# Performance work log

Hardware: AMD Instinct MI355X
Metric: run time of the kernel (lower is better)

Reference implementation:

```python
import jax, jax.numpy as jnp
import numpy as np

MAX_FPS = 30.0
NUM_HEADS = 8


def _rope(x, times):
    # x: [B, H, T, D] with D even; interleaved rotary (even/odd pairs)
    B, H, T, D = x.shape
    inv_freq = 1.0 / (10000.0 ** (jnp.arange(0, D, 2, dtype=jnp.float32) / D))  # [D/2]
    pos = jnp.round(times * MAX_FPS)                       # [B, T]
    freqs = pos[:, :, None] * inv_freq[None, None, :]      # [B, T, D/2]
    cos = jnp.cos(freqs)[:, None, :, :]                    # [B, 1, T, D/2]
    sin = jnp.sin(freqs)[:, None, :, :]
    xp = x.reshape(B, H, T, D // 2, 2)
    x0, x1 = xp[..., 0], xp[..., 1]                        # even-index, odd-index elems
    r0 = x0 * cos - x1 * sin
    r1 = x0 * sin + x1 * cos
    return jnp.stack([r0, r1], axis=-1).reshape(B, H, T, D)


def setup_inputs() -> dict:
    key = jax.random.key(0)
    k1, k2, k3, k4, k5 = jax.random.split(key, 5)
    B, N, C = 4, 2048, 512
    x = jax.random.normal(k1, (B, N, C), dtype=jnp.float32)
    mask = jnp.zeros((B, N), dtype=jnp.float32)  # additive mask, 0 = attend
    # times in seconds; rounded to frame indices inside RoPE
    times = jax.random.uniform(k2, (B, N), dtype=jnp.float32) * (N / MAX_FPS)
    bound_qkv = float(np.sqrt(6.0 / (C + 3 * C)))
    Wqkv = jax.random.uniform(k3, (3 * C, C), minval=-bound_qkv, maxval=bound_qkv, dtype=jnp.float32)
    bound_p = float(np.sqrt(6.0 / (C + C)))
    Wproj = jax.random.uniform(k4, (C, C), minval=-bound_p, maxval=bound_p, dtype=jnp.float32)
    bproj = jnp.zeros((C,), dtype=jnp.float32)
    return {"x": x, "mask": mask, "times": times, "Wqkv": Wqkv,
            "Wproj": Wproj, "bproj": bproj, "num_cls_token": 0}


def reference(x, mask, times, Wqkv, Wproj, bproj, num_cls_token):
    B, N, C = x.shape
    H = NUM_HEADS
    Dh = C // H
    qkv = (x @ Wqkv.T).reshape(B, N, 3, H, Dh).transpose(2, 0, 3, 1, 4)  # [3,B,H,N,Dh]
    q, k, v = qkv[0], qkv[1], qkv[2]
    if num_cls_token > 0:
        c_q, q = q[:, :, :num_cls_token], q[:, :, num_cls_token:]
        c_k, k = k[:, :, :num_cls_token], k[:, :, num_cls_token:]
        t = times
        q = _rope(q, t)
        k = _rope(k, t)
        q = jnp.concatenate([c_q, q], axis=2)
        k = jnp.concatenate([c_k, k], axis=2)
    else:
        q = _rope(q, times)
        k = _rope(k, times)
    scale = 1.0 / jnp.sqrt(jnp.float32(Dh))
    scores = jnp.einsum('bhqd,bhkd->bhqk', q, k) * scale + mask[:, None, None, :]
    attn = jax.nn.softmax(scores, axis=-1)
    out = jnp.einsum('bhqk,bhkd->bhqd', attn, v)           # [B,H,N,Dh]
    out = out.transpose(0, 2, 1, 3).reshape(B, N, C)
    return out @ Wproj.T + bproj
```

## Files before the change

kernel.cpp:

```cpp
#include <hip/hip_runtime.h>
#include <math.h>

#define BB 4
#define NN 2048
#define CC 512
#define HH 8
#define DH 64
#define MM (BB*NN)
#define QKV_N (3*CC)

typedef _Float16 f16;
typedef __attribute__((ext_vector_type(4))) _Float16 f16x4;
typedef __attribute__((ext_vector_type(8))) _Float16 f16x8;
typedef __attribute__((ext_vector_type(4))) float f32x4;

#define L2E 1.4426950408889634f

#define GL16(g, l) __builtin_amdgcn_global_load_lds(                       \
    (const __attribute__((address_space(1))) void*)(g),                    \
    (__attribute__((address_space(3))) void*)(l), 16, 0, 0)

#define SX4 (MM*CC/4)
#define SW4 (QKV_N*CC/4)
#define SP4 (CC*CC/4)
__global__ __launch_bounds__(256) void cast_kernel(
    const float* __restrict__ x, const float* __restrict__ wqkv,
    const float* __restrict__ wproj,
    f16* __restrict__ xh, f16* __restrict__ wqh, f16* __restrict__ wph)
{
    const int t = blockIdx.x * 256 + threadIdx.x;
    const float* src; f16* dst; int i;
    if (t < SX4)            { src = x;     dst = xh;  i = t; }
    else if (t < SX4 + SW4) { src = wqkv;  dst = wqh; i = t - SX4; }
    else                    { src = wproj; dst = wph; i = t - SX4 - SW4; }
    f32x4 v = *(const f32x4*)(src + 4 * (size_t)i);
    f16x4 h = { (f16)v[0], (f16)v[1], (f16)v[2], (f16)v[3] };
    *(f16x4*)(dst + 4 * (size_t)i) = h;
}

__global__ __launch_bounds__(256) void qkv_gemm(
    const f16* __restrict__ xh, const f16* __restrict__ wh,
    f16* __restrict__ qo, f16* __restrict__ ko, f16* __restrict__ vto)
{
    __shared__ f16 As[128][32];
    __shared__ f16 Bs[128][32];
    const int m0 = blockIdx.x * 128;
    const int n0 = blockIdx.y * 128;
    const int tid = threadIdx.x;
    const int lane = tid & 63;
    const int w = tid >> 6;
    const int wm = (w & 1) * 64, wn = (w >> 1) * 64;
    const int l15 = lane & 15, quad = lane >> 4;

    const int sr = tid >> 2;
    const int sc = (tid & 3) * 8;
    const f16* ga0 = xh + (size_t)(m0 + sr) * CC + sc;
    const f16* ga1 = xh + (size_t)(m0 + sr + 64) * CC + sc;
    const f16* gb0 = wh + (size_t)(n0 + sr) * CC + sc;
    const f16* gb1 = wh + (size_t)(n0 + sr + 64) * CC + sc;
    f16* la0 = &As[sr][sc];      f16* la1 = &As[sr + 64][sc];
    f16* lb0 = &Bs[sr][sc];      f16* lb1 = &Bs[sr + 64][sc];

    f32x4 acc[4][4] = {};
    for (int k0 = 0; k0 < CC; k0 += 32) {
        __syncthreads();
        GL16(ga0 + k0, la0);
        GL16(ga1 + k0, la1);
        GL16(gb0 + k0, lb0);
        GL16(gb1 + k0, lb1);
        __syncthreads();

        f16x8 af[4], bf[4];
        #pragma unroll
        for (int mi = 0; mi < 4; ++mi)
            af[mi] = *(const f16x8*)&As[wm + mi*16 + l15][quad * 8];
        #pragma unroll
        for (int ni = 0; ni < 4; ++ni)
            bf[ni] = *(const f16x8*)&Bs[wn + ni*16 + l15][quad * 8];
        #pragma unroll
        for (int mi = 0; mi < 4; ++mi)
            #pragma unroll
            for (int ni = 0; ni < 4; ++ni)
                acc[mi][ni] = __builtin_amdgcn_mfma_f32_16x16x32_f16(
                    af[mi], bf[ni], acc[mi][ni], 0, 0, 0);
    }

    const int which = n0 >> 9;
    const int b     = m0 >> 11;
    const int mloc  = m0 & (NN - 1);

    if (which == 2) {
        #pragma unroll
        for (int mi = 0; mi < 4; ++mi)
            #pragma unroll
            for (int ni = 0; ni < 4; ++ni) {
                const int cl = wn + ni*16 + l15;
                const int hh = ((n0 & 511) + cl) >> 6;
                const int d  = ((n0 & 511) + cl) & 63;
                const int n  = mloc + wm + mi*16 + quad*4;
                f16x4 pk = { (f16)acc[mi][ni][0], (f16)acc[mi][ni][1],
                             (f16)acc[mi][ni][2], (f16)acc[mi][ni][3] };
                *(f16x4*)(vto + ((size_t)(b*HH + hh) * DH + d) * NN + n) = pk;
            }
        return;
    }

    f16* dst = which ? ko : qo;
    #pragma unroll
    for (int mi = 0; mi < 4; ++mi)
        #pragma unroll
        for (int r = 0; r < 4; ++r) {
            const int n = mloc + wm + mi*16 + quad*4 + r;
            #pragma unroll
            for (int ni = 0; ni < 4; ++ni) {
                const int cl = wn + ni*16 + l15;
                const int hh = ((n0 & 511) + cl) >> 6;
                const int d  = ((n0 & 511) + cl) & 63;
                dst[((size_t)(b*HH + hh) * NN + n) * DH + d] = (f16)acc[mi][ni][r];
            }
        }
}

__global__ __launch_bounds__(256) void rope_kernel(
    f16* __restrict__ q, f16* __restrict__ k,
    const float* __restrict__ times, const int* __restrict__ nclsp)
{
    const int t = blockIdx.x * 256 + threadIdx.x;
    const int row = t >> 3;
    const int d0  = (t & 7) * 8;
    const int n   = row & (NN - 1);
    const int b   = row >> 14;
    if (n < *nclsp) return;
    const float pos = rintf(times[b * NN + n] * 30.0f);

    f16x8 qv = *(const f16x8*)(q + (size_t)row * DH + d0);
    f16x8 kv = *(const f16x8*)(k + (size_t)row * DH + d0);
    f16x8 qr, kr;
    #pragma unroll
    for (int p = 0; p < 4; ++p) {
        const int j = (d0 >> 1) + p;
        const float invf = exp2f((float)j * (-13.287712379549449f / 32.0f));
        float s, c;
        sincosf(pos * invf, &s, &c);
        const float q0 = (float)qv[2*p], q1 = (float)qv[2*p+1];
        qr[2*p]   = (f16)(q0 * c - q1 * s);
        qr[2*p+1] = (f16)(q0 * s + q1 * c);
        const float k0 = (float)kv[2*p], k1 = (float)kv[2*p+1];
        kr[2*p]   = (f16)(k0 * c - k1 * s);
        kr[2*p+1] = (f16)(k0 * s + k1 * c);
    }
    *(f16x8*)(q + (size_t)row * DH + d0) = qr;
    *(f16x8*)(k + (size_t)row * DH + d0) = kr;
}

__global__ __launch_bounds__(256, 2) void attn_kernel(
    const f16* __restrict__ qg, const f16* __restrict__ kg,
    const f16* __restrict__ vtg, const float* __restrict__ mask,
    f16* __restrict__ out)
{
    __shared__ f16 Kh[64][64];
    __shared__ f16 Vt[64][64];
    __shared__ float Msk[64];

    const int bh = blockIdx.x;
    const int qt = blockIdx.y;
    const int b = bh >> 3, h = bh & 7;
    const int tid = threadIdx.x;
    const int w = tid >> 6, lane = tid & 63;
    const int l15 = lane & 15, quad = lane >> 4;
    const int rho = l15 & 7;

    const f16* qbase  = qg  + ((size_t)bh * NN + qt*128 + w*32) * DH;
    const f16* kbase  = kg  + (size_t)bh * NN * DH;
    const f16* vtbase = vtg + (size_t)bh * DH * NN;
    const float* mbase = mask + (size_t)b * NN;

    f16x8 Bq[2][2];
    #pragma unroll
    for (int ni = 0; ni < 2; ++ni)
        #pragma unroll
        for (int kc = 0; kc < 2; ++kc)
            Bq[ni][kc] = *(const f16x8*)(qbase + (size_t)(16*ni + l15) * DH
                                         + kc*32 + quad*8);

    const f16x4 Aones = (l15 == 0) ? f16x4{1.0f16, 1.0f16, 1.0f16, 1.0f16}
                                   : f16x4{0.0f16, 0.0f16, 0.0f16, 0.0f16};

    f32x4 O[2][4] = {};
    f32x4 Lacc[2] = {};
    float m_run[2] = { -INFINITY, -INFINITY };
    const float scl = 0.125f * L2E;

    const int srr = tid >> 3;
    const int scb = tid & 7;
    const int sw  = (scb ^ (srr & 7)) * 8;

    for (int kt = 0; kt < 32; ++kt) {
        __syncthreads();
        f16x8 k0 = *(const f16x8*)(kbase + (size_t)(kt*64 + srr) * DH + scb*8);
        f16x8 k1 = *(const f16x8*)(kbase + (size_t)(kt*64 + srr + 32) * DH + scb*8);
        f16x8 v0 = *(const f16x8*)(vtbase + (size_t)srr * NN + kt*64 + scb*8);
        f16x8 v1 = *(const f16x8*)(vtbase + (size_t)(srr + 32) * NN + kt*64 + scb*8);
        *(f16x8*)&Kh[srr][sw]      = k0;
        *(f16x8*)&Kh[srr + 32][sw] = k1;
        *(f16x8*)&Vt[srr][sw]      = v0;
        *(f16x8*)&Vt[srr + 32][sw] = v1;
        if (tid < 16) {
            f32x4 mv = *(const f32x4*)(mbase + kt*64 + (tid << 2));
            mv *= L2E;
            *(f32x4*)&Msk[tid << 2] = mv;
        }
        __syncthreads();

        f32x4 st[4][2] = {};
        const int aw = (quad ^ rho) * 8;
        #pragma unroll
        for (int mi = 0; mi < 4; ++mi) {
            f16x8 Ak0 = *(const f16x8*)&Kh[16*mi + l15][aw];
            f16x8 Ak1 = *(const f16x8*)&Kh[16*mi + l15][aw ^ 32];
            #pragma unroll
            for (int ni = 0; ni < 2; ++ni) {
                st[mi][ni] = __builtin_amdgcn_mfma_f32_16x16x32_f16(Ak0, Bq[ni][0], st[mi][ni], 0, 0, 0);
                st[mi][ni] = __builtin_amdgcn_mfma_f32_16x16x32_f16(Ak1, Bq[ni][1], st[mi][ni], 0, 0, 0);
            }
        }

        f32x4 mskv[4];
        #pragma unroll
        for (int mi = 0; mi < 4; ++mi)
            mskv[mi] = *(const f32x4*)&Msk[16*mi + quad*4];

        f16x4 ph[4][2];
        float alpha[2];
        #pragma unroll
        for (int ni = 0; ni < 2; ++ni) {
            float mloc = -INFINITY;
            #pragma unroll
            for (int mi = 0; mi < 4; ++mi)
                #pragma unroll
                for (int r = 0; r < 4; ++r) {
                    float s2 = st[mi][ni][r] * scl + mskv[mi][r];
                    st[mi][ni][r] = s2;
                    mloc = fmaxf(mloc, s2);
                }
            mloc = fmaxf(mloc, __shfl_xor(mloc, 16));
            mloc = fmaxf(mloc, __shfl_xor(mloc, 32));
            const float mnew = fmaxf(m_run[ni], mloc);
            alpha[ni] = exp2f(m_run[ni] - mnew);
            m_run[ni] = mnew;
            #pragma unroll
            for (int mi = 0; mi < 4; ++mi)
                #pragma unroll
                for (int r = 0; r < 4; ++r)
                    ph[mi][ni][r] = (f16)exp2f(st[mi][ni][r] - mnew);
            #pragma unroll
            for (int nd = 0; nd < 4; ++nd)
                O[ni][nd] *= alpha[ni];
            Lacc[ni] *= alpha[ni];
        }

        #pragma unroll
        for (int mi = 0; mi < 4; ++mi) {
            Lacc[0] = __builtin_amdgcn_mfma_f32_16x16x16f16(Aones, ph[mi][0], Lacc[0], 0, 0, 0);
            Lacc[1] = __builtin_amdgcn_mfma_f32_16x16x16f16(Aones, ph[mi][1], Lacc[1], 0, 0, 0);
            #pragma unroll
            for (int nd = 0; nd < 4; ++nd) {
                const int vb = ((2*mi + (quad >> 1)) ^ rho) * 8 + (quad & 1) * 4;
                f16x4 Av = *(const f16x4*)&Vt[16*nd + l15][vb];
                O[0][nd] = __builtin_amdgcn_mfma_f32_16x16x16f16(Av, ph[mi][0], O[0][nd], 0, 0, 0);
                O[1][nd] = __builtin_amdgcn_mfma_f32_16x16x16f16(Av, ph[mi][1], O[1][nd], 0, 0, 0);
            }
        }
    }

    #pragma unroll
    for (int ni = 0; ni < 2; ++ni) {
        const float l = __shfl(Lacc[ni][0], l15);
        const float inv = 1.0f / l;
        const int qrow = qt*128 + w*32 + 16*ni + l15;
        f16* obase = out + ((size_t)b * NN + qrow) * CC + h * DH;
        #pragma unroll
        for (int nd = 0; nd < 4; ++nd) {
            f32x4 o = O[ni][nd] * inv;
            f16x4 oh = { (f16)o[0], (f16)o[1], (f16)o[2], (f16)o[3] };
            *(f16x4*)(obase + 16*nd + quad*4) = oh;
        }
    }
}

__global__ __launch_bounds__(256) void proj_gemm(
    const f16* __restrict__ ah, const f16* __restrict__ wh,
    const float* __restrict__ bias, float* __restrict__ out)
{
    __shared__ f16 As[128][32];
    __shared__ f16 Bs[128][32];
    const int m0 = blockIdx.x * 128;
    const int n0 = blockIdx.y * 128;
    const int tid = threadIdx.x;
    const int lane = tid & 63;
    const int w = tid >> 6;
    const int wm = (w & 1) * 64, wn = (w >> 1) * 64;
    const int l15 = lane & 15, quad = lane >> 4;

    const int sr = tid >> 2;
    const int sc = (tid & 3) * 8;
    const f16* ga0 = ah + (size_t)(m0 + sr) * CC + sc;
    const f16* ga1 = ah + (size_t)(m0 + sr + 64) * CC + sc;
    const f16* gb0 = wh + (size_t)(n0 + sr) * CC + sc;
    const f16* gb1 = wh + (size_t)(n0 + sr + 64) * CC + sc;
    f16* la0 = &As[sr][sc];      f16* la1 = &As[sr + 64][sc];
    f16* lb0 = &Bs[sr][sc];      f16* lb1 = &Bs[sr + 64][sc];

    f32x4 acc[4][4] = {};
    for (int k0 = 0; k0 < CC; k0 += 32) {
        __syncthreads();
        GL16(ga0 + k0, la0);
        GL16(ga1 + k0, la1);
        GL16(gb0 + k0, lb0);
        GL16(gb1 + k0, lb1);
        __syncthreads();

        f16x8 af[4], bf[4];
        #pragma unroll
        for (int mi = 0; mi < 4; ++mi)
            af[mi] = *(const f16x8*)&As[wm + mi*16 + l15][quad * 8];
        #pragma unroll
        for (int ni = 0; ni < 4; ++ni)
            bf[ni] = *(const f16x8*)&Bs[wn + ni*16 + l15][quad * 8];
        #pragma unroll
        for (int mi = 0; mi < 4; ++mi)
            #pragma unroll
            for (int ni = 0; ni < 4; ++ni)
                acc[mi][ni] = __builtin_amdgcn_mfma_f32_16x16x32_f16(
                    af[mi], bf[ni], acc[mi][ni], 0, 0, 0);
    }

    float bb[4];
    #pragma unroll
    for (int ni = 0; ni < 4; ++ni)
        bb[ni] = bias[n0 + wn + ni*16 + l15];

    #pragma unroll
    for (int mi = 0; mi < 4; ++mi)
        #pragma unroll
        for (int r = 0; r < 4; ++r) {
            const int m = m0 + wm + mi*16 + quad*4 + r;
            #pragma unroll
            for (int ni = 0; ni < 4; ++ni)
                out[(size_t)m * CC + n0 + wn + ni*16 + l15] = acc[mi][ni][r] + bb[ni];
        }
}

extern "C" void kernel_launch(void* const* d_in, const int* in_sizes, int n_in,
                              void* d_out, int out_size, void* d_ws, size_t ws_size,
                              hipStream_t stream)
{
    const float* x     = (const float*)d_in[0];
    const float* mask  = (const float*)d_in[1];
    const float* times = (const float*)d_in[2];
    const float* Wqkv  = (const float*)d_in[3];
    const float* Wproj = (const float*)d_in[4];
    const float* bproj = (const float*)d_in[5];
    const int*   ncls  = (const int*)d_in[6];
    float* out = (float*)d_out;

    const size_t per = (size_t)BB * HH * NN * DH;
    f16* xh  = (f16*)d_ws;
    f16* wqh = xh + per;
    f16* wph = wqh + (size_t)QKV_N * CC;
    f16* q   = wph + (size_t)CC * CC;
    f16* k   = q + per;
    f16* vt  = k + per;
    f16* ao  = vt + per;

    cast_kernel<<<(SX4 + SW4 + SP4) / 256, 256, 0, stream>>>(
        x, Wqkv, Wproj, xh, wqh, wph);
    qkv_gemm<<<dim3(MM / 128, QKV_N / 128), 256, 0, stream>>>(
        xh, wqh, q, k, vt);
    rope_kernel<<<(MM * HH * DH / 8) / 256, 256, 0, stream>>>(
        q, k, times, ncls);
    attn_kernel<<<dim3(BB * HH, NN / 128), 256, 0, stream>>>(
        q, k, vt, mask, ao);
    proj_gemm<<<dim3(MM / 128, CC / 128), 256, 0, stream>>>(
        ao, wph, bproj, out);
}
```

Before: 198.8 us.

## Fuse RoPE into QKV GEMM epilogue, pre-swizzle K/V tiles, double-buffer attention loads

The QKV GEMM epilogue now stages its accumulators through shared memory and applies RoPE there, which removes the separate rope kernel and its global read-modify-write of Q and K. K and V are written in a pre-swizzled per-64-row tile layout, so the attention kernel can double-buffer them with direct global-to-LDS loads and overlap the next tile's fetch with compute. The attention kernel also reads the mask straight from global into registers and skips rescaling the O accumulators when no running max in the wave changed. The projection GEMM switches to 128x64 tiles to launch more blocks, at the cost of more redundant A-tile loads.

```diff
diff --git a/kernel.cpp b/kernel.cpp
--- a/kernel.cpp
+++ b/kernel.cpp
@@ -40,10 +40,13 @@
 
 __global__ __launch_bounds__(256) void qkv_gemm(
     const f16* __restrict__ xh, const f16* __restrict__ wh,
-    f16* __restrict__ qo, f16* __restrict__ ko, f16* __restrict__ vto)
+    const float* __restrict__ times, const int* __restrict__ nclsp,
+    f16* __restrict__ qo, f16* __restrict__ ksw, f16* __restrict__ vsw)
 {
-    __shared__ f16 As[128][32];
-    __shared__ f16 Bs[128][32];
+    __shared__ __align__(16) char smem[16896];
+    f16 (*As)[32] = (f16 (*)[32])smem;
+    f16 (*Bs)[32] = (f16 (*)[32])(smem + 8192);
+
     const int m0 = blockIdx.x * 128;
     const int n0 = blockIdx.y * 128;
     const int tid = threadIdx.x;
@@ -84,95 +87,117 @@
                 acc[mi][ni] = __builtin_amdgcn_mfma_f32_16x16x32_f16(
                     af[mi], bf[ni], acc[mi][ni], 0, 0, 0);
     }
+    __syncthreads();
 
     const int which = n0 >> 9;
     const int b     = m0 >> 11;
     const int mloc  = m0 & (NN - 1);
-
-    if (which == 2) {
-        #pragma unroll
-        for (int mi = 0; mi < 4; ++mi)
-            #pragma unroll
-            for (int ni = 0; ni < 4; ++ni) {
-                const int cl = wn + ni*16 + l15;
-                const int hh = ((n0 & 511) + cl) >> 6;
-                const int d  = ((n0 & 511) + cl) & 63;
-                const int n  = mloc + wm + mi*16 + quad*4;
-                f16x4 pk = { (f16)acc[mi][ni][0], (f16)acc[mi][ni][1],
-                             (f16)acc[mi][ni][2], (f16)acc[mi][ni][3] };
-                *(f16x4*)(vto + ((size_t)(b*HH + hh) * DH + d) * NN + n) = pk;
-            }
+    const int hbase = (n0 & 511) >> 6;
+
+    if (which < 2) {
+        f16 (*Tr)[132] = (f16 (*)[132])smem;
+        const int ncls = *nclsp;
+        #pragma unroll
+        for (int c = 0; c < 2; ++c) {
+            if ((w & 1) == c) {
+                #pragma unroll
+                for (int mi = 0; mi < 4; ++mi)
+                    #pragma unroll
+                    for (int ni = 0; ni < 4; ++ni)
+                        #pragma unroll
+                        for (int r = 0; r < 4; ++r)
+                            Tr[16*mi + quad*4 + r][wn + 16*ni + l15] =
+                                (f16)acc[mi][ni][r];
+            }
+            __syncthreads();
+            const int row = tid >> 2, cg = tid & 3;
+            const int n   = mloc + c*64 + row;
+            const int hh  = hbase + (cg >> 1);
+            const int d0  = (cg & 1) * 32;
+            f16x8 vv[4];
+            #pragma unroll
+            for (int j = 0; j < 4; ++j)
+                vv[j] = *(const f16x8*)&Tr[row][cg*32 + j*8];
+            if (n >= ncls) {
+                const float pos = rintf(times[(size_t)b*NN + n] * 30.0f);
+                #pragma unroll
+                for (int j = 0; j < 4; ++j)
+                    #pragma unroll
+                    for (int p = 0; p < 4; ++p) {
+                        const int fi = (d0 >> 1) + j*4 + p;
+                        const float invf =
+                            exp2f((float)fi * (-13.287712379549449f / 32.0f));
+                        float s, co; sincosf(pos * invf, &s, &co);
+                        const float x0 = (float)vv[j][2*p];
+                        const float x1 = (float)vv[j][2*p+1];
+                        vv[j][2*p]   = (f16)(x0*co - x1*s);
+                        vv[j][2*p+1] = (f16)(x0*s + x1*co);
+                    }
+            }
+            if (which == 0) {
+                f16* qp = qo + (((size_t)(b*HH + hh))*NN + n)*DH + d0;
+                #pragma unroll
+                for (int j = 0; j < 4; ++j)
+                    *(f16x8*)(qp + 8*j) = vv[j];
+            } else {
+                const int ktile = (mloc >> 6) + c;
+                f16* kp = ksw + ((((size_t)(b*HH + hh))*32 + ktile)*64 + row)*64;
+                #pragma unroll
+                for (int j = 0; j < 4; ++j) {
+                    const int blk = (d0 >> 3) + j;
+                    *(f16x8*)(kp + ((blk ^ (row & 7)) * 8)) = vv[j];
+                }
+            }
+            if (c == 0) __syncthreads();
+        }
         return;
     }
 
-    f16* dst = which ? ko : qo;
+    f16 (*Tv)[66] = (f16 (*)[66])smem;
     #pragma unroll
-    for (int mi = 0; mi < 4; ++mi)
-        #pragma unroll
-        for (int r = 0; r < 4; ++r) {
-            const int n = mloc + wm + mi*16 + quad*4 + r;
-            #pragma unroll
-            for (int ni = 0; ni < 4; ++ni) {
-                const int cl = wn + ni*16 + l15;
-                const int hh = ((n0 & 511) + cl) >> 6;
-                const int d  = ((n0 & 511) + cl) & 63;
-                dst[((size_t)(b*HH + hh) * NN + n) * DH + d] = (f16)acc[mi][ni][r];
-            }
-        }
+    for (int c = 0; c < 2; ++c) {
+        if ((w & 1) == c) {
+            #pragma unroll
+            for (int mi = 0; mi < 4; ++mi)
+                #pragma unroll
+                for (int ni = 0; ni < 4; ++ni) {
+                    f16x4 pk = { (f16)acc[mi][ni][0], (f16)acc[mi][ni][1],
+                                 (f16)acc[mi][ni][2], (f16)acc[mi][ni][3] };
+                    *(f16x4*)&Tv[wn + 16*ni + l15][16*mi + quad*4] = pk;
+                }
+        }
+        __syncthreads();
+        const int rr = tid >> 1;
+        const int d  = rr & 63, hh = hbase + (rr >> 6);
+        const int ktile = (mloc >> 6) + c;
+        f16* vp = vsw + ((((size_t)(b*HH + hh))*32 + ktile)*64 + d)*64;
+        #pragma unroll
+        for (int j = 0; j < 4; ++j) {
+            const int blk = (tid & 1)*4 + j;
+            f16x8 t = *(const f16x8*)&Tv[rr][(tid & 1)*32 + j*8];
+            *(f16x8*)(vp + ((blk ^ (d & 7)) * 8)) = t;
+        }
+        if (c == 0) __syncthreads();
+    }
 }
 
-__global__ __launch_bounds__(256) void rope_kernel(
-    f16* __restrict__ q, f16* __restrict__ k,
-    const float* __restrict__ times, const int* __restrict__ nclsp)
-{
-    const int t = blockIdx.x * 256 + threadIdx.x;
-    const int row = t >> 3;
-    const int d0  = (t & 7) * 8;
-    const int n   = row & (NN - 1);
-    const int b   = row >> 14;
-    if (n < *nclsp) return;
-    const float pos = rintf(times[b * NN + n] * 30.0f);
-
-    f16x8 qv = *(const f16x8*)(q + (size_t)row * DH + d0);
-    f16x8 kv = *(const f16x8*)(k + (size_t)row * DH + d0);
-    f16x8 qr, kr;
-    #pragma unroll
-    for (int p = 0; p < 4; ++p) {
-        const int j = (d0 >> 1) + p;
-        const float invf = exp2f((float)j * (-13.287712379549449f / 32.0f));
-        float s, c;
-        sincosf(pos * invf, &s, &c);
-        const float q0 = (float)qv[2*p], q1 = (float)qv[2*p+1];
-        qr[2*p]   = (f16)(q0 * c - q1 * s);
-        qr[2*p+1] = (f16)(q0 * s + q1 * c);
-        const float k0 = (float)kv[2*p], k1 = (float)kv[2*p+1];
-        kr[2*p]   = (f16)(k0 * c - k1 * s);
-        kr[2*p+1] = (f16)(k0 * s + k1 * c);
-    }
-    *(f16x8*)(q + (size_t)row * DH + d0) = qr;
-    *(f16x8*)(k + (size_t)row * DH + d0) = kr;
-}
-
 __global__ __launch_bounds__(256, 2) void attn_kernel(
-    const f16* __restrict__ qg, const f16* __restrict__ kg,
-    const f16* __restrict__ vtg, const float* __restrict__ mask,
+    const f16* __restrict__ qg, const f16* __restrict__ ksw,
+    const f16* __restrict__ vsw, const float* __restrict__ mask,
     f16* __restrict__ out)
 {
-    __shared__ f16 Kh[64][64];
-    __shared__ f16 Vt[64][64];
-    __shared__ float Msk[64];
-
-    const int bh = blockIdx.x;
-    const int qt = blockIdx.y;
+    __shared__ __align__(16) f16 asm_[4][4096];
+
+    const int bh = blockIdx.x, qt = blockIdx.y;
     const int b = bh >> 3, h = bh & 7;
     const int tid = threadIdx.x;
     const int w = tid >> 6, lane = tid & 63;
     const int l15 = lane & 15, quad = lane >> 4;
     const int rho = l15 & 7;
 
-    const f16* qbase  = qg  + ((size_t)bh * NN + qt*128 + w*32) * DH;
-    const f16* kbase  = kg  + (size_t)bh * NN * DH;
-    const f16* vtbase = vtg + (size_t)bh * DH * NN;
+    const f16* qbase = qg + ((size_t)bh * NN + qt*128 + w*32) * DH;
+    const f16* kt0 = ksw + (size_t)bh * 32 * 4096;
+    const f16* vt0 = vsw + (size_t)bh * 32 * 4096;
     const float* mbase = mask + (size_t)b * NN;
 
     f16x8 Bq[2][2];
@@ -191,26 +216,36 @@
     float m_run[2] = { -INFINITY, -INFINITY };
     const float scl = 0.125f * L2E;
 
-    const int srr = tid >> 3;
-    const int scb = tid & 7;
-    const int sw  = (scb ^ (srr & 7)) * 8;
+    {
+        const f16* ks = kt0 + tid*8;
+        const f16* vs = vt0 + tid*8;
+        GL16(ks,        &asm_[0][tid*8]);
+        GL16(ks + 2048, &asm_[0][2048 + tid*8]);
+        GL16(vs,        &asm_[1][tid*8]);
+        GL16(vs + 2048, &asm_[1][2048 + tid*8]);
+    }
 
     for (int kt = 0; kt < 32; ++kt) {
-        __syncthreads();
-        f16x8 k0 = *(const f16x8*)(kbase + (size_t)(kt*64 + srr) * DH + scb*8);
-        f16x8 k1 = *(const f16x8*)(kbase + (size_t)(kt*64 + srr + 32) * DH + scb*8);
-        f16x8 v0 = *(const f16x8*)(vtbase + (size_t)srr * NN + kt*64 + scb*8);
-        f16x8 v1 = *(const f16x8*)(vtbase + (size_t)(srr + 32) * NN + kt*64 + scb*8);
-        *(f16x8*)&Kh[srr][sw]      = k0;
-        *(f16x8*)&Kh[srr + 32][sw] = k1;
-        *(f16x8*)&Vt[srr][sw]      = v0;
-        *(f16x8*)&Vt[srr + 32][sw] = v1;
-        if (tid < 16) {
-            f32x4 mv = *(const f32x4*)(mbase + kt*64 + (tid << 2));
-            mv *= L2E;
-            *(f32x4*)&Msk[tid << 2] = mv;
-        }
-        __syncthreads();
+        const int cur = (kt & 1) * 2;
+        __syncthreads();
+        if (kt + 1 < 32) {
+            const int nxt = 2 - cur;
+            const f16* ks = kt0 + (size_t)(kt+1)*4096 + tid*8;
+            const f16* vs = vt0 + (size_t)(kt+1)*4096 + tid*8;
+            GL16(ks,        &asm_[nxt][tid*8]);
+            GL16(ks + 2048, &asm_[nxt][2048 + tid*8]);
+            GL16(vs,        &asm_[nxt+1][tid*8]);
+            GL16(vs + 2048, &asm_[nxt+1][2048 + tid*8]);
+        }
+        const f16 (*Kh)[64] = (const f16 (*)[64])asm_[cur];
+        const f16 (*Vt)[64] = (const f16 (*)[64])asm_[cur + 1];
+
+        f32x4 mskv[4];
+        #pragma unroll
+        for (int mi = 0; mi < 4; ++mi) {
+            f32x4 mv = *(const f32x4*)(mbase + kt*64 + 16*mi + quad*4);
+            mskv[mi] = mv * L2E;
+        }
 
         f32x4 st[4][2] = {};
         const int aw = (quad ^ rho) * 8;
@@ -225,27 +260,24 @@
             }
         }
 
-        f32x4 mskv[4];
-        #pragma unroll
-        for (int mi = 0; mi < 4; ++mi)
-            mskv[mi] = *(const f32x4*)&Msk[16*mi + quad*4];
-
         f16x4 ph[4][2];
         float alpha[2];
+        bool upd = false;
         #pragma unroll
         for (int ni = 0; ni < 2; ++ni) {
-            float mloc = -INFINITY;
+            float mloc2 = -INFINITY;
             #pragma unroll
             for (int mi = 0; mi < 4; ++mi)
                 #pragma unroll
                 for (int r = 0; r < 4; ++r) {
                     float s2 = st[mi][ni][r] * scl + mskv[mi][r];
                     st[mi][ni][r] = s2;
-                    mloc = fmaxf(mloc, s2);
+                    mloc2 = fmaxf(mloc2, s2);
                 }
-            mloc = fmaxf(mloc, __shfl_xor(mloc, 16));
-            mloc = fmaxf(mloc, __shfl_xor(mloc, 32));
-            const float mnew = fmaxf(m_run[ni], mloc);
+            mloc2 = fmaxf(mloc2, __shfl_xor(mloc2, 16));
+            mloc2 = fmaxf(mloc2, __shfl_xor(mloc2, 32));
+            const float mnew = fmaxf(m_run[ni], mloc2);
+            upd |= (mnew > m_run[ni]);
             alpha[ni] = exp2f(m_run[ni] - mnew);
             m_run[ni] = mnew;
             #pragma unroll
@@ -253,10 +285,15 @@
                 #pragma unroll
                 for (int r = 0; r < 4; ++r)
                     ph[mi][ni][r] = (f16)exp2f(st[mi][ni][r] - mnew);
-            #pragma unroll
-            for (int nd = 0; nd < 4; ++nd)
-                O[ni][nd] *= alpha[ni];
-            Lacc[ni] *= alpha[ni];
+        }
+        if (__any((int)upd)) {
+            #pragma unroll
+            for (int ni = 0; ni < 2; ++ni) {
+                #pragma unroll
+                for (int nd = 0; nd < 4; ++nd)
+                    O[ni][nd] *= alpha[ni];
+                Lacc[ni] *= alpha[ni];
+            }
         }
 
         #pragma unroll
@@ -293,13 +330,13 @@
     const float* __restrict__ bias, float* __restrict__ out)
 {
     __shared__ f16 As[128][32];
-    __shared__ f16 Bs[128][32];
+    __shared__ f16 Bs[64][32];
     const int m0 = blockIdx.x * 128;
-    const int n0 = blockIdx.y * 128;
+    const int n0 = blockIdx.y * 64;
     const int tid = threadIdx.x;
     const int lane = tid & 63;
     const int w = tid >> 6;
-    const int wm = (w & 1) * 64, wn = (w >> 1) * 64;
+    const int wm = (w & 1) * 64, wn = (w >> 1) * 32;
     const int l15 = lane & 15, quad = lane >> 4;
 
     const int sr = tid >> 2;
@@ -307,37 +344,35 @@
     const f16* ga0 = ah + (size_t)(m0 + sr) * CC + sc;
     const f16* ga1 = ah + (size_t)(m0 + sr + 64) * CC + sc;
     const f16* gb0 = wh + (size_t)(n0 + sr) * CC + sc;
-    const f16* gb1 = wh + (size_t)(n0 + sr + 64) * CC + sc;
     f16* la0 = &As[sr][sc];      f16* la1 = &As[sr + 64][sc];
-    f16* lb0 = &Bs[sr][sc];      f16* lb1 = &Bs[sr + 64][sc];
-
-    f32x4 acc[4][4] = {};
+    f16* lb0 = &Bs[sr][sc];
+
+    f32x4 acc[4][2] = {};
     for (int k0 = 0; k0 < CC; k0 += 32) {
         __syncthreads();
         GL16(ga0 + k0, la0);
         GL16(ga1 + k0, la1);
         GL16(gb0 + k0, lb0);
-        GL16(gb1 + k0, lb1);
-        __syncthreads();
-
-        f16x8 af[4], bf[4];
+        __syncthreads();
+
+        f16x8 af[4], bf[2];
         #pragma unroll
         for (int mi = 0; mi < 4; ++mi)
             af[mi] = *(const f16x8*)&As[wm + mi*16 + l15][quad * 8];
         #pragma unroll
-        for (int ni = 0; ni < 4; ++ni)
+        for (int ni = 0; ni < 2; ++ni)
             bf[ni] = *(const f16x8*)&Bs[wn + ni*16 + l15][quad * 8];
         #pragma unroll
         for (int mi = 0; mi < 4; ++mi)
             #pragma unroll
-            for (int ni = 0; ni < 4; ++ni)
+            for (int ni = 0; ni < 2; ++ni)
                 acc[mi][ni] = __builtin_amdgcn_mfma_f32_16x16x32_f16(
                     af[mi], bf[ni], acc[mi][ni], 0, 0, 0);
     }
 
-    float bb[4];
+    float bb[2];
     #pragma unroll
-    for (int ni = 0; ni < 4; ++ni)
+    for (int ni = 0; ni < 2; ++ni)
         bb[ni] = bias[n0 + wn + ni*16 + l15];
 
     #pragma unroll
@@ -346,7 +381,7 @@
         for (int r = 0; r < 4; ++r) {
             const int m = m0 + wm + mi*16 + quad*4 + r;
             #pragma unroll
-            for (int ni = 0; ni < 4; ++ni)
+            for (int ni = 0; ni < 2; ++ni)
                 out[(size_t)m * CC + n0 + wn + ni*16 + l15] = acc[mi][ni][r] + bb[ni];
         }
 }
@@ -369,18 +404,16 @@
     f16* wqh = xh + per;
     f16* wph = wqh + (size_t)QKV_N * CC;
     f16* q   = wph + (size_t)CC * CC;
-    f16* k   = q + per;
-    f16* vt  = k + per;
-    f16* ao  = vt + per;
+    f16* ks  = q + per;
+    f16* vs  = ks + per;
+    f16* ao  = vs + per;
 
     cast_kernel<<<(SX4 + SW4 + SP4) / 256, 256, 0, stream>>>(
         x, Wqkv, Wproj, xh, wqh, wph);
     qkv_gemm<<<dim3(MM / 128, QKV_N / 128), 256, 0, stream>>>(
-        xh, wqh, q, k, vt);
-    rope_kernel<<<(MM * HH * DH / 8) / 256, 256, 0, stream>>>(
-        q, k, times, ncls);
+        xh, wqh, times, ncls, q, ks, vs);
     attn_kernel<<<dim3(BB * HH, NN / 128), 256, 0, stream>>>(
-        q, k, vt, mask, ao);
-    proj_gemm<<<dim3(MM / 128, CC / 128), 256, 0, stream>>>(
+        q, ks, vs, mask, ao);
+    proj_gemm<<<dim3(MM / 128, CC / 64), 256, 0, stream>>>(
         ao, wph, bproj, out);
 }
```

Result: slower. 206.9 us (+4.1%).
